# Kernel optimization log

Measured on AMD Instinct MI355X. Metric: run time of the kernel, lower is better.

## Reference

```python
import jax, jax.numpy as jnp
import numpy as np

N = 20000      # nodes
IN = 256       # in_dim
OUT = 128      # out_dim
S = 8          # num_sect
K = S + 1      # sectors + self branch
EP = 40000     # edges per sector


def setup_inputs() -> dict:
    key = jax.random.key(0)
    ks = jax.random.split(key, 10)
    x = jax.random.normal(ks[0], (N, IN), jnp.float32)
    rows = jax.random.randint(ks[1], (S, EP), 0, N)  # src (adj row)
    cols = jax.random.randint(ks[2], (S, EP), 0, N)  # dst (adj col)
    # degree norms (buffers derived from the graph, as in compute_norm)
    out_deg = np.bincount(np.asarray(rows).ravel(), minlength=N).astype(np.float32)
    in_deg = np.bincount(np.asarray(cols).ravel(), minlength=N).astype(np.float32)
    out_norm = jnp.asarray(np.clip(out_deg, 1.0, None) ** -0.5)[:, None]  # [N,1]
    in_norm = jnp.asarray(np.clip(in_deg, 1.0, None) ** -0.5)[:, None]    # [N,1]
    s = 0.05  # xavier-ish scale
    W_self = jax.random.normal(ks[3], (IN, OUT), jnp.float32) * s
    W_sect = jax.random.normal(ks[4], (S, IN, OUT), jnp.float32) * s
    WC = jax.random.normal(ks[5], (OUT, OUT), jnp.float32) * s
    WD = jax.random.normal(ks[6], (OUT, OUT), jnp.float32) * s
    gate_w = jax.random.normal(ks[7], (2 * K * OUT, 1), jnp.float32) * s
    gate_b = jnp.zeros((1,), jnp.float32)
    return {"x": x, "W_self": W_self, "W_sect": W_sect, "WC": WC, "WD": WD,
            "gate_w": gate_w, "gate_b": gate_b, "out_norm": out_norm,
            "in_norm": in_norm, "rows": rows, "cols": cols}


def reference(x, W_self, W_sect, WC, WD, gate_w, gate_b, out_norm, in_norm, rows, cols):
    n = x.shape[0]
    # --- forward_sector_agg (dropout is identity in eval / drop_rate=0) ---
    z_self = x @ W_self                                    # [N, OUT]
    H = jnp.einsum('ni,sio->sno', x, W_sect) * out_norm    # [S, N, OUT]
    def agg(h, r, c):  # sparse adj @ h : z[src] += h[dst]
        return jax.ops.segment_sum(h[c], r, num_segments=n)
    Z = jax.vmap(agg)(H, rows, cols)                       # [S, N, OUT]
    z = jnp.concatenate([z_self[None], Z], axis=0)         # [K, N, OUT]
    z = jnp.transpose(z, (1, 0, 2)) * in_norm[:, :, None]  # [N, K, OUT]
    # --- heter_sen_interaction ---
    zc = z @ WC                                            # [N, K, D]
    com = jnp.einsum('nkd,njd->nkj', zc, zc)
    ac = jax.nn.softmax(com, axis=2)
    z_com = jnp.einsum('nkj,njd->nkd', ac, zc).reshape(n, -1)
    zd = z @ WD
    sub = zd[:, :, None, :] - zd[:, None, :, :]            # [N, K, K, D]
    ds = jnp.einsum('nkd,nkjd->nkj', zd, sub)
    ad = jax.nn.softmax(ds, axis=2)
    z_dis = jnp.einsum('nkj,nkjd->nkd', ad, sub).reshape(n, -1)
    cat = jnp.concatenate([z_com, z_dis], axis=-1)         # [N, 2*K*D]
    beta = jax.nn.sigmoid(cat @ gate_w + gate_b)           # [N, 1]
    return beta * z_com + (1.0 - beta) * z_dis             # [N, K*D]
```

## Files before the change

### kernel.cpp

```cpp
#include <hip/hip_runtime.h>
#include <math.h>

#define N_NODES 20000
#define IN_DIM  256
#define OUT_DIM 128
#define S_SECT  8
#define K_BR    9
#define NK      (K_BR*OUT_DIM)
#define EP_EDGE 40000
#define N_EDGES (S_SECT*EP_EDGE)
#define N_BINS  (S_SECT*N_NODES)
#define SCAN_BLOCKS 160
#define M_ROWS  (N_NODES*K_BR)
#define ZP      136
#define TP      136

typedef float v4f __attribute__((ext_vector_type(4)));
typedef short v8s __attribute__((ext_vector_type(8)));

__device__ inline unsigned short f2bf(float f) {
  union { float f; unsigned u; } v; v.f = f;
  unsigned r = v.u + 0x7fff + ((v.u >> 16) & 1);
  return (unsigned short)(r >> 16);
}
__device__ inline float bf2f(unsigned short h) {
  union { unsigned u; float f; } v; v.u = ((unsigned)h) << 16;
  return v.f;
}

__global__ __launch_bounds__(256) void k_prep(
    const float* __restrict__ Wself, const float* __restrict__ Wsect,
    const float* __restrict__ WC, const float* __restrict__ WD,
    unsigned short* __restrict__ Wtg, unsigned short* __restrict__ Btg)
{
  const int id = blockIdx.x * 256 + threadIdx.x;
  if (id < NK*IN_DIM) {
    const int j = id >> 8, k = id & 255;
    float w;
    if (j < OUT_DIM) w = Wself[(size_t)k*OUT_DIM + j];
    else {
      const int s = (j - OUT_DIM) >> 7, c = (j - OUT_DIM) & 127;
      w = Wsect[(size_t)s*(IN_DIM*OUT_DIM) + (size_t)k*OUT_DIM + c];
    }
    Wtg[id] = f2bf(w);
  } else {
    const int id2 = id - NK*IN_DIM;
    if (id2 < 256*128) {
      const int n = id2 >> 7, k = id2 & 127;
      const float w = (n < OUT_DIM) ? WC[k*OUT_DIM + n] : WD[k*OUT_DIM + (n - OUT_DIM)];
      Btg[id2] = f2bf(w);
    }
  }
}

__global__ __launch_bounds__(256, 4) void k_gemm_xw_mfma(
    const float* __restrict__ x, const unsigned short* __restrict__ Wtg,
    const float* __restrict__ outn, const float* __restrict__ inn,
    unsigned short* __restrict__ Hbuf, unsigned short* __restrict__ Zbufh)
{
  __shared__ unsigned short Bls[128*ZP];
  const int t = threadIdx.x;
  const int wave = t >> 6, lane = t & 63;
  const int mrow = lane & 15, quad = lane >> 4;
  const int m0 = blockIdx.x * 64 + wave * 16;

  v8s afr[8];
  {
    const int r = m0 + mrow;
    const bool ok = (r < N_NODES);
    const float* src = x + (size_t)r*IN_DIM + quad*8;
    #pragma unroll
    for (int kq = 0; kq < 8; ++kq) {
      float4 a0 = {0.f,0.f,0.f,0.f}, a1 = {0.f,0.f,0.f,0.f};
      if (ok) {
        a0 = *(const float4*)(src + kq*32);
        a1 = *(const float4*)(src + kq*32 + 4);
      }
      v8s f;
      f[0] = (short)f2bf(a0.x); f[1] = (short)f2bf(a0.y);
      f[2] = (short)f2bf(a0.z); f[3] = (short)f2bf(a0.w);
      f[4] = (short)f2bf(a1.x); f[5] = (short)f2bf(a1.y);
      f[6] = (short)f2bf(a1.z); f[7] = (short)f2bf(a1.w);
      afr[kq] = f;
    }
  }

  for (int jj = 0; jj < 3; ++jj) {
    const int jb = blockIdx.y * 3 + jj;

    v4f acc[8];
    #pragma unroll
    for (int jt = 0; jt < 8; ++jt) acc[jt] = (v4f){0.f,0.f,0.f,0.f};

    for (int kh = 0; kh < 2; ++kh) {
      #pragma unroll
      for (int i = 0; i < 8; ++i) {
        const int idx = t + i*256;
        const int row = idx >> 4, c8 = idx & 15;
        *(uint4*)(Bls + row*ZP + c8*8) =
            *(const uint4*)(Wtg + (size_t)(jb*128 + row)*IN_DIM + kh*128 + c8*8);
      }
      __syncthreads();

      #pragma unroll
      for (int kq = 0; kq < 4; ++kq) {
        #pragma unroll
        for (int jt = 0; jt < 8; ++jt) {
          const v8s bf = *(const v8s*)(Bls + (jt*16 + mrow)*ZP + kq*32 + quad*8);
          acc[jt] = __builtin_amdgcn_mfma_f32_16x16x32_bf16(afr[kh*4 + kq], bf, acc[jt], 0, 0, 0);
        }
      }
      __syncthreads();
    }

    if (jb == 0) {
      #pragma unroll
      for (int p = 0; p < 4; ++p) {
        const int R = m0 + quad*4 + p;
        if (R >= N_NODES) continue;
        const float iw = inn[R];
        #pragma unroll
        for (int jt = 0; jt < 8; ++jt)
          Zbufh[(size_t)R*NK + jt*16 + mrow] = f2bf(acc[jt][p] * iw);
      }
    } else {
      const int s = jb - 1;
      #pragma unroll
      for (int p = 0; p < 4; ++p) {
        const int R = m0 + quad*4 + p;
        if (R >= N_NODES) continue;
        const float ow = outn[R];
        #pragma unroll
        for (int jt = 0; jt < 8; ++jt)
          Hbuf[((size_t)s*N_NODES + R)*OUT_DIM + jt*16 + mrow] = f2bf(acc[jt][p] * ow);
      }
    }
  }
}

__global__ __launch_bounds__(256) void k_count(
    const int* __restrict__ rows, int* __restrict__ cnt)
{
  const int id = blockIdx.x * 256 + threadIdx.x;
  if (id >= N_EDGES) return;
  const int s = id / EP_EDGE;
  atomicAdd(&cnt[s * N_NODES + rows[id]], 1);
}

__global__ __launch_bounds__(256) void k_scan1(
    const int* __restrict__ cnt, int* __restrict__ bsum)
{
  __shared__ int sh[256];
  const int t = threadIdx.x;
  const int base = blockIdx.x * 1000;
  int s = 0;
  if (t < 250) {
    const int i = base + t*4;
    s = cnt[i] + cnt[i+1] + cnt[i+2] + cnt[i+3];
  }
  sh[t] = s; __syncthreads();
  for (int off = 128; off > 0; off >>= 1) {
    if (t < off) sh[t] += sh[t + off];
    __syncthreads();
  }
  if (t == 0) bsum[blockIdx.x] = sh[0];
}

__global__ void k_scan2(const int* __restrict__ bsum, int* __restrict__ boff)
{
  if (threadIdx.x == 0) {
    int acc = 0;
    for (int b = 0; b < SCAN_BLOCKS; ++b) { boff[b] = acc; acc += bsum[b]; }
  }
}

__global__ __launch_bounds__(256) void k_scan3(
    const int* __restrict__ cnt, const int* __restrict__ boff,
    int* __restrict__ offs)
{
  __shared__ int sh[256];
  const int t = threadIdx.x;
  const int base = blockIdx.x * 1000;
  int v[4] = {0,0,0,0};
  int mySum = 0;
  if (t < 250) {
    const int i = base + t*4;
    v[0]=cnt[i]; v[1]=cnt[i+1]; v[2]=cnt[i+2]; v[3]=cnt[i+3];
    mySum = v[0]+v[1]+v[2]+v[3];
  }
  sh[t] = mySum; __syncthreads();
  for (int off = 1; off < 256; off <<= 1) {
    int add = (t >= off) ? sh[t - off] : 0;
    __syncthreads();
    sh[t] += add;
    __syncthreads();
  }
  if (t < 250) {
    int excl = boff[blockIdx.x] + sh[t] - mySum;
    const int i = base + t*4;
    offs[i]   = excl;           excl += v[0];
    offs[i+1] = excl;           excl += v[1];
    offs[i+2] = excl;           excl += v[2];
    offs[i+3] = excl;
  }
}

__global__ __launch_bounds__(256) void k_scatter(
    const int* __restrict__ rows, const int* __restrict__ cols,
    const int* __restrict__ offs, int* __restrict__ cur,
    int* __restrict__ eCol)
{
  const int id = blockIdx.x * 256 + threadIdx.x;
  if (id >= N_EDGES) return;
  const int s = id / EP_EDGE;
  const int bin = s * N_NODES + rows[id];
  const int pos = offs[bin] + atomicAdd(&cur[bin], 1);
  eCol[pos] = cols[id];
}

__global__ __launch_bounds__(256) void k_agg_csr(
    const unsigned short* __restrict__ Hbuf, const int* __restrict__ offs,
    const int* __restrict__ cnt, const int* __restrict__ eCol,
    const float* __restrict__ inn, unsigned short* __restrict__ Zbufh)
{
  const long long tid = (long long)blockIdx.x * 256 + threadIdx.x;
  const int group = (int)(tid >> 5);
  if (group >= N_BINS) return;
  const int lane = (int)(tid & 31);
  const int s = group / N_NODES;
  const int r = group - s * N_NODES;
  const int start = offs[group];
  const int n = cnt[group];
  float4 acc = {0.f, 0.f, 0.f, 0.f};
  for (int i = 0; i < n; ++i) {
    const int c = eCol[start + i];
    const uint2 h = *(const uint2*)(Hbuf + ((size_t)s*N_NODES + c)*OUT_DIM + lane*4);
    acc.x += bf2f((unsigned short)h.x);
    acc.y += bf2f((unsigned short)(h.x >> 16));
    acc.z += bf2f((unsigned short)h.y);
    acc.w += bf2f((unsigned short)(h.y >> 16));
  }
  const float w = inn[r];
  uint2 o;
  o.x = (unsigned)f2bf(acc.x * w) | ((unsigned)f2bf(acc.y * w) << 16);
  o.y = (unsigned)f2bf(acc.z * w) | ((unsigned)f2bf(acc.w * w) << 16);
  *(uint2*)(Zbufh + ((size_t)r*K_BR + 1 + s)*OUT_DIM + lane*4) = o;
}

__global__ __launch_bounds__(256, 2) void k_zcd_interact(
    const unsigned short* __restrict__ Zbufh, const unsigned short* __restrict__ Btg,
    const float* __restrict__ gw, const float* __restrict__ gb,
    float* __restrict__ out)
{
  __shared__ unsigned short Bls[64*ZP];
  __shared__ unsigned short tls[8][2][9*TP];
  __shared__ float graw[8][2][K_BR][10];
  __shared__ float gs[8][2][K_BR][10];
  const int t = threadIdx.x;
  const int wv = t >> 6, lane = t & 63;
  const int mrow = lane & 15, quad = lane >> 4;
  const int n0 = blockIdx.x * 8;
  const int rowbase = (n0 + 2*wv)*9;

  v8s afr[2][4];
  #pragma unroll
  for (int rb = 0; rb < 2; ++rb) {
    const int rloc = rb*16 + mrow;
    const bool ok = (rloc < 18);
    const unsigned short* src = Zbufh + (size_t)(rowbase + rloc)*OUT_DIM + quad*8;
    #pragma unroll
    for (int kq = 0; kq < 4; ++kq) {
      v8s f = {0,0,0,0,0,0,0,0};
      if (ok) f = *(const v8s*)(src + kq*32);
      afr[rb][kq] = f;
    }
  }

  for (int jh = 0; jh < 2; ++jh) {
    v4f acc[2][8];
    #pragma unroll
    for (int rb = 0; rb < 2; ++rb)
      #pragma unroll
      for (int j = 0; j < 8; ++j) acc[rb][j] = (v4f){0.f,0.f,0.f,0.f};

    for (int sub = 0; sub < 2; ++sub) {
      #pragma unroll
      for (int i = 0; i < 4; ++i) {
        const int idx = t + i*256;
        const int row = idx >> 4, c8 = idx & 15;
        *(uint4*)(Bls + row*ZP + c8*8) =
            *(const uint4*)(Btg + (size_t)(jh*128 + sub*64 + row)*OUT_DIM + c8*8);
      }
      __syncthreads();
      #pragma unroll
      for (int jl = 0; jl < 4; ++jl) {
        const unsigned short* bp = Bls + (jl*16 + mrow)*ZP + quad*8;
        #pragma unroll
        for (int kq = 0; kq < 4; ++kq) {
          const v8s bf = *(const v8s*)(bp + kq*32);
          acc[0][sub*4+jl] = __builtin_amdgcn_mfma_f32_16x16x32_bf16(afr[0][kq], bf, acc[0][sub*4+jl], 0, 0, 0);
          acc[1][sub*4+jl] = __builtin_amdgcn_mfma_f32_16x16x32_bf16(afr[1][kq], bf, acc[1][sub*4+jl], 0, 0, 0);
        }
      }
      __syncthreads();
    }

    #pragma unroll
    for (int rb = 0; rb < 2; ++rb)
      #pragma unroll
      for (int p = 0; p < 4; ++p) {
        const int R = rb*16 + quad*4 + p;
        if (R >= 18) continue;
        const int nn = (R >= 9) ? 1 : 0;
        const int kk = R - nn*9;
        unsigned short* dst = &tls[wv*2 + nn][jh][kk*TP + mrow];
        #pragma unroll
        for (int jj = 0; jj < 8; ++jj)
          dst[jj*16] = f2bf(acc[rb][jj][p]);
      }
  }

  {
    const int r = lane & 15;
    #pragma unroll
    for (int q = 0; q < 4; ++q) {
      const int node = wv*2 + (q >> 1), mat = q & 1;
      const unsigned short* src = &tls[node][mat][r*TP + quad*8];
      v8s frag[4];
      #pragma unroll
      for (int kq = 0; kq < 4; ++kq) {
        v8s f = {0,0,0,0,0,0,0,0};
        if (r < K_BR) f = *(const v8s*)(src + kq*32);
        frag[kq] = f;
      }
      v4f acc = {0.f,0.f,0.f,0.f};
      #pragma unroll
      for (int kq = 0; kq < 4; ++kq)
        acc = __builtin_amdgcn_mfma_f32_16x16x32_bf16(frag[kq], frag[kq], acc, 0, 0, 0);
      if (r < K_BR) {
        #pragma unroll
        for (int p = 0; p < 4; ++p) {
          const int m = quad*4 + p;
          if (m < K_BR) graw[node][mat][m][r] = acc[p];
        }
      }
    }
  }

  if (lane < 36) {
    const int nn2  = (lane >= 18) ? 1 : 0;
    const int node = wv*2 + nn2;
    const int rem  = lane - nn2*18;
    const int mat  = (rem >= 9) ? 1 : 0;
    const int k    = rem - mat*9;
    float v[9];
    if (mat == 0) {
      #pragma unroll
      for (int j = 0; j < 9; ++j) v[j] = graw[node][0][k][j];
    } else {
      const float gkk = graw[node][1][k][k];
      #pragma unroll
      for (int j = 0; j < 9; ++j) v[j] = gkk - graw[node][1][k][j];
    }
    float m = v[0];
    #pragma unroll
    for (int j = 1; j < 9; ++j) m = fmaxf(m, v[j]);
    float sum = 0.f;
    #pragma unroll
    for (int j = 0; j < 9; ++j) { v[j] = expf(v[j] - m); sum += v[j]; }
    const float inv = 1.f / sum;
    #pragma unroll
    for (int j = 0; j < 9; ++j) gs[node][mat][k][j] = v[j] * inv;
  }

  const float gbv = gb[0];
  float gwc[2][9], gwd[2][9];
  #pragma unroll
  for (int dd = 0; dd < 2; ++dd) {
    const int d = lane + dd*64;
    #pragma unroll
    for (int j = 0; j < 9; ++j) {
      gwc[dd][j] = gw[j*OUT_DIM + d];
      gwd[dd][j] = gw[NK + j*OUT_DIM + d];
    }
  }

  for (int nn = 0; nn < 2; ++nn) {
    const int node = wv*2 + nn;
    float zcj[2][9], zdj[2][9];
    #pragma unroll
    for (int dd = 0; dd < 2; ++dd) {
      const int d = lane + dd*64;
      #pragma unroll
      for (int j = 0; j < 9; ++j) {
        zcj[dd][j] = bf2f(tls[node][0][j*TP + d]);
        zdj[dd][j] = bf2f(tls[node][1][j*TP + d]);
      }
    }
    float zcomK[2][9], zdisK[2][9];
    float gp = 0.f;
    #pragma unroll
    for (int k = 0; k < 9; ++k) {
      #pragma unroll
      for (int dd = 0; dd < 2; ++dd) {
        float zc = 0.f, ad = 0.f;
        #pragma unroll
        for (int j = 0; j < 9; ++j) {
          zc += gs[node][0][k][j] * zcj[dd][j];
          ad += gs[node][1][k][j] * zdj[dd][j];
        }
        zcomK[dd][k] = zc;
        zdisK[dd][k] = zdj[dd][k] - ad;
        gp += zc * gwc[dd][k] + zdisK[dd][k] * gwd[dd][k];
      }
    }
    #pragma unroll
    for (int off = 32; off > 0; off >>= 1) gp += __shfl_xor(gp, off, 64);
    const float beta = 1.f / (1.f + expf(-(gp + gbv)));
    #pragma unroll
    for (int k = 0; k < 9; ++k) {
      #pragma unroll
      for (int dd = 0; dd < 2; ++dd) {
        const int d = lane + dd*64;
        out[(size_t)(n0+node)*NK + k*OUT_DIM + d] =
            beta*zcomK[dd][k] + (1.f-beta)*zdisK[dd][k];
      }
    }
  }
}

extern "C" void kernel_launch(void* const* d_in, const int* in_sizes, int n_in,
                              void* d_out, int out_size, void* d_ws, size_t ws_size,
                              hipStream_t stream)
{
  const float* x     = (const float*)d_in[0];
  const float* Wself = (const float*)d_in[1];
  const float* Wsect = (const float*)d_in[2];
  const float* WC    = (const float*)d_in[3];
  const float* WD    = (const float*)d_in[4];
  const float* gw    = (const float*)d_in[5];
  const float* gb    = (const float*)d_in[6];
  const float* outn  = (const float*)d_in[7];
  const float* inn   = (const float*)d_in[8];
  const int*   rows  = (const int*)d_in[9];
  const int*   cols  = (const int*)d_in[10];
  float* out = (float*)d_out;

  char* p = (char*)d_ws;
  unsigned short* Hbuf  = (unsigned short*)p; p += (size_t)S_SECT*N_NODES*OUT_DIM*2;
  unsigned short* Zbufh = (unsigned short*)p; p += (size_t)M_ROWS*OUT_DIM*2;
  int* cnt    = (int*)p;                      p += (size_t)N_BINS*4;
  int* offs   = (int*)p;                      p += (size_t)N_BINS*4;
  int* cur    = (int*)p;                      p += (size_t)N_BINS*4;
  int* bsum   = (int*)p;                      p += 256*4;
  int* boff   = (int*)p;                      p += 256*4;
  int* eCol   = (int*)p;                      p += (size_t)N_EDGES*4;
  unsigned short* Btg = (unsigned short*)p;   p += 256*128*2;
  unsigned short* Wtg = (unsigned short*)p;   p += (size_t)NK*IN_DIM*2;

  hipMemsetAsync(cnt, 0, (size_t)N_BINS*4, stream);
  hipMemsetAsync(cur, 0, (size_t)N_BINS*4, stream);

  k_prep<<<(NK*IN_DIM + 256*128 + 255)/256, 256, 0, stream>>>(Wself, Wsect, WC, WD, Wtg, Btg);

  dim3 gA((N_NODES + 63)/64, 3);
  k_gemm_xw_mfma<<<gA, 256, 0, stream>>>(x, Wtg, outn, inn, Hbuf, Zbufh);

  const int eb = (N_EDGES + 255)/256;
  k_count  <<<eb, 256, 0, stream>>>(rows, cnt);
  k_scan1  <<<SCAN_BLOCKS, 256, 0, stream>>>(cnt, bsum);
  k_scan2  <<<1, 64, 0, stream>>>(bsum, boff);
  k_scan3  <<<SCAN_BLOCKS, 256, 0, stream>>>(cnt, boff, offs);
  k_scatter<<<eb, 256, 0, stream>>>(rows, cols, offs, cur, eCol);

  const int aggBlocks = (N_BINS*32 + 255)/256;
  k_agg_csr<<<aggBlocks, 256, 0, stream>>>(Hbuf, offs, cnt, eCol, inn, Zbufh);

  k_zcd_interact<<<N_NODES/8, 256, 0, stream>>>(Zbufh, Btg, gw, gb, out);
}
```

Baseline: 298.4 us.

## Read WC/WD weights directly from global memory and transpose MFMA operands

The per-block staging of the concatenated WC/WD weight tile through shared memory, along with its two __syncthreads per sub-tile, is removed. B fragments are now loaded straight from global memory (expected to be cache-resident) into the MFMA. The MFMA operand order is swapped so each lane holds four contiguous output columns, which lets the results go to the shared tile as packed 8-byte stores instead of scattered 2-byte stores. Dropping the shared buffer and raising launch bounds to 3 blocks per CU aims at higher occupancy, at the cost of repeated global/L2 weight reads and tighter register limits.

```diff
diff --git a/kernel.cpp b/kernel.cpp
--- a/kernel.cpp
+++ b/kernel.cpp
@@ -247,12 +247,11 @@
   *(uint2*)(Zbufh + ((size_t)r*K_BR + 1 + s)*OUT_DIM + lane*4) = o;
 }
 
-__global__ __launch_bounds__(256, 2) void k_zcd_interact(
+__global__ __launch_bounds__(256, 3) void k_zcd_interact(
     const unsigned short* __restrict__ Zbufh, const unsigned short* __restrict__ Btg,
     const float* __restrict__ gw, const float* __restrict__ gb,
     float* __restrict__ out)
 {
-  __shared__ unsigned short Bls[64*ZP];
   __shared__ unsigned short tls[8][2][9*TP];
   __shared__ float graw[8][2][K_BR][10];
   __shared__ float gs[8][2][K_BR][10];
@@ -283,41 +282,33 @@
       #pragma unroll
       for (int j = 0; j < 8; ++j) acc[rb][j] = (v4f){0.f,0.f,0.f,0.f};
 
-    for (int sub = 0; sub < 2; ++sub) {
-      #pragma unroll
-      for (int i = 0; i < 4; ++i) {
-        const int idx = t + i*256;
-        const int row = idx >> 4, c8 = idx & 15;
-        *(uint4*)(Bls + row*ZP + c8*8) =
-            *(const uint4*)(Btg + (size_t)(jh*128 + sub*64 + row)*OUT_DIM + c8*8);
-      }
-      __syncthreads();
-      #pragma unroll
-      for (int jl = 0; jl < 4; ++jl) {
-        const unsigned short* bp = Bls + (jl*16 + mrow)*ZP + quad*8;
-        #pragma unroll
-        for (int kq = 0; kq < 4; ++kq) {
-          const v8s bf = *(const v8s*)(bp + kq*32);
-          acc[0][sub*4+jl] = __builtin_amdgcn_mfma_f32_16x16x32_bf16(afr[0][kq], bf, acc[0][sub*4+jl], 0, 0, 0);
-          acc[1][sub*4+jl] = __builtin_amdgcn_mfma_f32_16x16x32_bf16(afr[1][kq], bf, acc[1][sub*4+jl], 0, 0, 0);
+    #pragma unroll
+    for (int j = 0; j < 8; ++j) {
+      const unsigned short* bp = Btg + (size_t)(jh*128 + j*16 + mrow)*OUT_DIM + quad*8;
+      #pragma unroll
+      for (int kq = 0; kq < 4; ++kq) {
+        const v8s bf = *(const v8s*)(bp + kq*32);
+        acc[0][j] = __builtin_amdgcn_mfma_f32_16x16x32_bf16(bf, afr[0][kq], acc[0][j], 0, 0, 0);
+        acc[1][j] = __builtin_amdgcn_mfma_f32_16x16x32_bf16(bf, afr[1][kq], acc[1][j], 0, 0, 0);
+      }
+    }
+
+    #pragma unroll
+    for (int rb = 0; rb < 2; ++rb) {
+      const int m = rb*16 + mrow;
+      if (m < 18) {
+        const int nn = (m >= 9) ? 1 : 0;
+        const int kk = m - nn*9;
+        unsigned short* dst = &tls[wv*2 + nn][jh][kk*TP];
+        #pragma unroll
+        for (int j = 0; j < 8; ++j) {
+          uint2 o;
+          o.x = (unsigned)f2bf(acc[rb][j][0]) | ((unsigned)f2bf(acc[rb][j][1]) << 16);
+          o.y = (unsigned)f2bf(acc[rb][j][2]) | ((unsigned)f2bf(acc[rb][j][3]) << 16);
+          *(uint2*)(dst + j*16 + quad*4) = o;
         }
       }
-      __syncthreads();
-    }
-
-    #pragma unroll
-    for (int rb = 0; rb < 2; ++rb)
-      #pragma unroll
-      for (int p = 0; p < 4; ++p) {
-        const int R = rb*16 + quad*4 + p;
-        if (R >= 18) continue;
-        const int nn = (R >= 9) ? 1 : 0;
-        const int kk = R - nn*9;
-        unsigned short* dst = &tls[wv*2 + nn][jh][kk*TP + mrow];
-        #pragma unroll
-        for (int jj = 0; jj < 8; ++jj)
-          dst[jj*16] = f2bf(acc[rb][jj][p]);
-      }
+    }
   }
 
   {
```

Result: slower. 328.1 us (+9.9%).

## Assign one node per wavefront in interaction kernel with 512-thread blocks

Applied to the files above, without the earlier changes.

The interaction kernel now runs 8 wavefronts per block, each handling a single node instead of two. The MFMA operands are swapped so each lane holds four consecutive output columns, which allows packed 8-byte LDS stores instead of scattered 2-byte ones. This halves per-wave accumulator registers and serial work, giving more parallelism and cheaper tile writes. In exchange, 16-row MFMA tiles with only 9 valid rows waste more MFMA lanes, and the larger block raises per-block LDS and sync cost.

```diff
diff --git a/kernel.cpp b/kernel.cpp
--- a/kernel.cpp
+++ b/kernel.cpp
@@ -247,7 +247,7 @@
   *(uint2*)(Zbufh + ((size_t)r*K_BR + 1 + s)*OUT_DIM + lane*4) = o;
 }
 
-__global__ __launch_bounds__(256, 2) void k_zcd_interact(
+__global__ __launch_bounds__(512, 4) void k_zcd_interact(
     const unsigned short* __restrict__ Zbufh, const unsigned short* __restrict__ Btg,
     const float* __restrict__ gw, const float* __restrict__ gb,
     float* __restrict__ out)
@@ -260,33 +260,29 @@
   const int wv = t >> 6, lane = t & 63;
   const int mrow = lane & 15, quad = lane >> 4;
   const int n0 = blockIdx.x * 8;
-  const int rowbase = (n0 + 2*wv)*9;
-
-  v8s afr[2][4];
-  #pragma unroll
-  for (int rb = 0; rb < 2; ++rb) {
-    const int rloc = rb*16 + mrow;
-    const bool ok = (rloc < 18);
-    const unsigned short* src = Zbufh + (size_t)(rowbase + rloc)*OUT_DIM + quad*8;
+  const int rowbase = (n0 + wv)*9;
+
+  v8s afr[4];
+  {
+    const bool ok = (mrow < 9);
+    const unsigned short* src = Zbufh + (size_t)(rowbase + mrow)*OUT_DIM + quad*8;
     #pragma unroll
     for (int kq = 0; kq < 4; ++kq) {
       v8s f = {0,0,0,0,0,0,0,0};
       if (ok) f = *(const v8s*)(src + kq*32);
-      afr[rb][kq] = f;
+      afr[kq] = f;
     }
   }
 
   for (int jh = 0; jh < 2; ++jh) {
-    v4f acc[2][8];
-    #pragma unroll
-    for (int rb = 0; rb < 2; ++rb)
-      #pragma unroll
-      for (int j = 0; j < 8; ++j) acc[rb][j] = (v4f){0.f,0.f,0.f,0.f};
+    v4f acc[8];
+    #pragma unroll
+    for (int j = 0; j < 8; ++j) acc[j] = (v4f){0.f,0.f,0.f,0.f};
 
     for (int sub = 0; sub < 2; ++sub) {
       #pragma unroll
-      for (int i = 0; i < 4; ++i) {
-        const int idx = t + i*256;
+      for (int i = 0; i < 2; ++i) {
+        const int idx = t + i*512;
         const int row = idx >> 4, c8 = idx & 15;
         *(uint4*)(Bls + row*ZP + c8*8) =
             *(const uint4*)(Btg + (size_t)(jh*128 + sub*64 + row)*OUT_DIM + c8*8);
@@ -298,34 +294,30 @@
         #pragma unroll
         for (int kq = 0; kq < 4; ++kq) {
           const v8s bf = *(const v8s*)(bp + kq*32);
-          acc[0][sub*4+jl] = __builtin_amdgcn_mfma_f32_16x16x32_bf16(afr[0][kq], bf, acc[0][sub*4+jl], 0, 0, 0);
-          acc[1][sub*4+jl] = __builtin_amdgcn_mfma_f32_16x16x32_bf16(afr[1][kq], bf, acc[1][sub*4+jl], 0, 0, 0);
+          acc[sub*4+jl] = __builtin_amdgcn_mfma_f32_16x16x32_bf16(bf, afr[kq], acc[sub*4+jl], 0, 0, 0);
         }
       }
       __syncthreads();
     }
 
-    #pragma unroll
-    for (int rb = 0; rb < 2; ++rb)
-      #pragma unroll
-      for (int p = 0; p < 4; ++p) {
-        const int R = rb*16 + quad*4 + p;
-        if (R >= 18) continue;
-        const int nn = (R >= 9) ? 1 : 0;
-        const int kk = R - nn*9;
-        unsigned short* dst = &tls[wv*2 + nn][jh][kk*TP + mrow];
-        #pragma unroll
-        for (int jj = 0; jj < 8; ++jj)
-          dst[jj*16] = f2bf(acc[rb][jj][p]);
-      }
+    if (mrow < 9) {
+      unsigned short* dst = &tls[wv][jh][mrow*TP];
+      #pragma unroll
+      for (int a = 0; a < 8; ++a) {
+        const int off = (a >> 2)*64 + (a & 3)*16 + quad*4;
+        uint2 o;
+        o.x = (unsigned)f2bf(acc[a][0]) | ((unsigned)f2bf(acc[a][1]) << 16);
+        o.y = (unsigned)f2bf(acc[a][2]) | ((unsigned)f2bf(acc[a][3]) << 16);
+        *(uint2*)(dst + off) = o;
+      }
+    }
   }
 
   {
     const int r = lane & 15;
     #pragma unroll
-    for (int q = 0; q < 4; ++q) {
-      const int node = wv*2 + (q >> 1), mat = q & 1;
-      const unsigned short* src = &tls[node][mat][r*TP + quad*8];
+    for (int mat = 0; mat < 2; ++mat) {
+      const unsigned short* src = &tls[wv][mat][r*TP + quad*8];
       v8s frag[4];
       #pragma unroll
       for (int kq = 0; kq < 4; ++kq) {
@@ -341,26 +333,23 @@
         #pragma unroll
         for (int p = 0; p < 4; ++p) {
           const int m = quad*4 + p;
-          if (m < K_BR) graw[node][mat][m][r] = acc[p];
+          if (m < K_BR) graw[wv][mat][m][r] = acc[p];
         }
       }
     }
   }
 
-  if (lane < 36) {
-    const int nn2  = (lane >= 18) ? 1 : 0;
-    const int node = wv*2 + nn2;
-    const int rem  = lane - nn2*18;
-    const int mat  = (rem >= 9) ? 1 : 0;
-    const int k    = rem - mat*9;
+  if (lane < 18) {
+    const int mat = (lane >= 9) ? 1 : 0;
+    const int k   = lane - mat*9;
     float v[9];
     if (mat == 0) {
       #pragma unroll
-      for (int j = 0; j < 9; ++j) v[j] = graw[node][0][k][j];
+      for (int j = 0; j < 9; ++j) v[j] = graw[wv][0][k][j];
     } else {
-      const float gkk = graw[node][1][k][k];
-      #pragma unroll
-      for (int j = 0; j < 9; ++j) v[j] = gkk - graw[node][1][k][j];
+      const float gkk = graw[wv][1][k][k];
+      #pragma unroll
+      for (int j = 0; j < 9; ++j) v[j] = gkk - graw[wv][1][k][j];
     }
     float m = v[0];
     #pragma unroll
@@ -370,7 +359,7 @@
     for (int j = 0; j < 9; ++j) { v[j] = expf(v[j] - m); sum += v[j]; }
     const float inv = 1.f / sum;
     #pragma unroll
-    for (int j = 0; j < 9; ++j) gs[node][mat][k][j] = v[j] * inv;
+    for (int j = 0; j < 9; ++j) gs[wv][mat][k][j] = v[j] * inv;
   }
 
   const float gbv = gb[0];
@@ -385,46 +374,43 @@
     }
   }
 
-  for (int nn = 0; nn < 2; ++nn) {
-    const int node = wv*2 + nn;
-    float zcj[2][9], zdj[2][9];
+  float zcj[2][9], zdj[2][9];
+  #pragma unroll
+  for (int dd = 0; dd < 2; ++dd) {
+    const int d = lane + dd*64;
+    #pragma unroll
+    for (int j = 0; j < 9; ++j) {
+      zcj[dd][j] = bf2f(tls[wv][0][j*TP + d]);
+      zdj[dd][j] = bf2f(tls[wv][1][j*TP + d]);
+    }
+  }
+  float zcomK[2][9], zdisK[2][9];
+  float gp = 0.f;
+  #pragma unroll
+  for (int k = 0; k < 9; ++k) {
+    #pragma unroll
+    for (int dd = 0; dd < 2; ++dd) {
+      float zc = 0.f, ad = 0.f;
+      #pragma unroll
+      for (int j = 0; j < 9; ++j) {
+        zc += gs[wv][0][k][j] * zcj[dd][j];
+        ad += gs[wv][1][k][j] * zdj[dd][j];
+      }
+      zcomK[dd][k] = zc;
+      zdisK[dd][k] = zdj[dd][k] - ad;
+      gp += zc * gwc[dd][k] + zdisK[dd][k] * gwd[dd][k];
+    }
+  }
+  #pragma unroll
+  for (int off = 32; off > 0; off >>= 1) gp += __shfl_xor(gp, off, 64);
+  const float beta = 1.f / (1.f + expf(-(gp + gbv)));
+  #pragma unroll
+  for (int k = 0; k < 9; ++k) {
     #pragma unroll
     for (int dd = 0; dd < 2; ++dd) {
       const int d = lane + dd*64;
-      #pragma unroll
-      for (int j = 0; j < 9; ++j) {
-        zcj[dd][j] = bf2f(tls[node][0][j*TP + d]);
-        zdj[dd][j] = bf2f(tls[node][1][j*TP + d]);
-      }
-    }
-    float zcomK[2][9], zdisK[2][9];
-    float gp = 0.f;
-    #pragma unroll
-    for (int k = 0; k < 9; ++k) {
-      #pragma unroll
-      for (int dd = 0; dd < 2; ++dd) {
-        float zc = 0.f, ad = 0.f;
-        #pragma unroll
-        for (int j = 0; j < 9; ++j) {
-          zc += gs[node][0][k][j] * zcj[dd][j];
-          ad += gs[node][1][k][j] * zdj[dd][j];
-        }
-        zcomK[dd][k] = zc;
-        zdisK[dd][k] = zdj[dd][k] - ad;
-        gp += zc * gwc[dd][k] + zdisK[dd][k] * gwd[dd][k];
-      }
-    }
-    #pragma unroll
-    for (int off = 32; off > 0; off >>= 1) gp += __shfl_xor(gp, off, 64);
-    const float beta = 1.f / (1.f + expf(-(gp + gbv)));
-    #pragma unroll
-    for (int k = 0; k < 9; ++k) {
-      #pragma unroll
-      for (int dd = 0; dd < 2; ++dd) {
-        const int d = lane + dd*64;
-        out[(size_t)(n0+node)*NK + k*OUT_DIM + d] =
-            beta*zcomK[dd][k] + (1.f-beta)*zdisK[dd][k];
-      }
+      out[(size_t)(n0+wv)*NK + k*OUT_DIM + d] =
+          beta*zcomK[dd][k] + (1.f-beta)*zdisK[dd][k];
     }
   }
 }
@@ -476,5 +462,5 @@
   const int aggBlocks = (N_BINS*32 + 255)/256;
   k_agg_csr<<<aggBlocks, 256, 0, stream>>>(Hbuf, offs, cnt, eCol, inn, Zbufh);
 
-  k_zcd_interact<<<N_NODES/8, 256, 0, stream>>>(Zbufh, Btg, gw, gb, out);
-}
+  k_zcd_interact<<<N_NODES/8, 512, 0, stream>>>(Zbufh, Btg, gw, gb, out);
+}
```

Result: faster. 292.0 us (-2.2%).
